# Kernel tuning notes

Measured on AMD Instinct MI355X. Metric: run time of the kernel, lower is better.

## Reference

```python
import jax, jax.numpy as jnp
import numpy as np

N_NODES = 100000
N_PAIRS = 1600000
F = 64
H = 4
D = F // H  # head dim = 16


def setup_inputs() -> dict:
    key = jax.random.key(0)
    ks = jax.random.split(key, 9)
    x = jax.random.normal(ks[0], (N_NODES, F), dtype=jnp.float32)
    w_ij = jax.random.normal(ks[1], (N_PAIRS, F), dtype=jnp.float32)
    phi_r_cut = jax.random.uniform(ks[2], (N_PAIRS,), dtype=jnp.float32)
    pair_mask = jnp.ones((N_PAIRS,), dtype=jnp.float32)
    Wq = jax.random.normal(ks[3], (H, D, D), dtype=jnp.float32) / np.sqrt(D)
    Wk = jax.random.normal(ks[4], (H, D, D), dtype=jnp.float32) / np.sqrt(D)
    Wv = jax.random.normal(ks[5], (H, D, D), dtype=jnp.float32) / np.sqrt(D)
    idx_i = jnp.sort(jax.random.randint(ks[6], (N_PAIRS,), 0, N_NODES)).astype(jnp.int64)
    idx_j = jax.random.randint(ks[7], (N_PAIRS,), 0, N_NODES).astype(jnp.int64)
    return {"x": x, "w_ij": w_ij, "phi_r_cut": phi_r_cut, "pair_mask": pair_mask,
            "Wq": Wq, "Wk": Wk, "Wv": Wv, "idx_i": idx_i, "idx_j": idx_j}


def reference(x, w_ij, phi_r_cut, pair_mask, Wq, Wk, Wv, idx_i, idx_j):
    n, f = x.shape
    h, d, _ = Wq.shape
    xh = x.reshape(n, h, d)            # (n, H, D) head split
    wh = w_ij.reshape(-1, h, d)        # (p, H, D)
    # per-head projections (Dense with no bias: x @ kernel), then gather by edge
    q_i = jnp.einsum('nhd,hde->nhe', xh, Wq)[idx_i]   # (p, H, D)
    k_j = jnp.einsum('nhd,hde->nhe', xh, Wk)[idx_j]   # (p, H, D)
    alpha = (q_i * wh * k_j).sum(axis=-1) / jnp.sqrt(jnp.asarray(d, x.dtype))  # (p, H)
    alpha = alpha * (pair_mask * phi_r_cut)[:, None]  # safe_scale with cutoff * mask
    v_j = jnp.einsum('nhd,hde->nhe', xh, Wv)[idx_j]   # (p, H, D)
    out = jax.ops.segment_sum(alpha[..., None] * v_j, idx_i, num_segments=n)  # (n, H, D)
    return out.reshape(n, f)
```

## Files before the change

kernel.cpp:

```cpp
#include <hip/hip_runtime.h>
#include <stdint.h>

#define N_NODES_C 100000
#define N_PAIRS_C 1600000
#define FDIM 64
#define HH 4
#define DD 16

__global__ __launch_bounds__(256) void qkv_kernel(
    const float* __restrict__ x,
    const float* __restrict__ Wq,
    const float* __restrict__ Wk,
    const float* __restrict__ Wv,
    float* __restrict__ q,
    float* __restrict__ k,
    float* __restrict__ v)
{
    __shared__ float sWq[HH * DD * DD];
    __shared__ float sWk[HH * DD * DD];
    __shared__ float sWv[HH * DD * DD];
    for (int t = threadIdx.x; t < HH * DD * DD; t += 256) {
        sWq[t] = Wq[t];
        sWk[t] = Wk[t];
        sWv[t] = Wv[t];
    }
    __syncthreads();

    int gid = blockIdx.x * 256 + threadIdx.x;
    int n = gid >> 2;
    int h = gid & 3;
    if (n >= N_NODES_C) return;

    const float* xp = x + (int64_t)n * FDIM + h * DD;
    float xr[DD];
#pragma unroll
    for (int d0 = 0; d0 < DD; d0 += 4) {
        float4 t4 = *reinterpret_cast<const float4*>(xp + d0);
        xr[d0 + 0] = t4.x; xr[d0 + 1] = t4.y; xr[d0 + 2] = t4.z; xr[d0 + 3] = t4.w;
    }

    float qo[DD], ko[DD], vo[DD];
#pragma unroll
    for (int e = 0; e < DD; e++) { qo[e] = 0.f; ko[e] = 0.f; vo[e] = 0.f; }

    const float* wqh = sWq + h * DD * DD;
    const float* wkh = sWk + h * DD * DD;
    const float* wvh = sWv + h * DD * DD;
#pragma unroll
    for (int d = 0; d < DD; d++) {
        float xv = xr[d];
#pragma unroll
        for (int e = 0; e < DD; e++) {
            qo[e] = fmaf(xv, wqh[d * DD + e], qo[e]);
            ko[e] = fmaf(xv, wkh[d * DD + e], ko[e]);
            vo[e] = fmaf(xv, wvh[d * DD + e], vo[e]);
        }
    }

    int64_t base = (int64_t)n * FDIM + h * DD;
#pragma unroll
    for (int e0 = 0; e0 < DD; e0 += 4) {
        *reinterpret_cast<float4*>(q + base + e0) = make_float4(qo[e0], qo[e0+1], qo[e0+2], qo[e0+3]);
        *reinterpret_cast<float4*>(k + base + e0) = make_float4(ko[e0], ko[e0+1], ko[e0+2], ko[e0+3]);
        *reinterpret_cast<float4*>(v + base + e0) = make_float4(vo[e0], vo[e0+1], vo[e0+2], vo[e0+3]);
    }
}

__global__ __launch_bounds__(256) void pair_kernel(
    const float* __restrict__ q,
    const float* __restrict__ k,
    const float* __restrict__ v,
    const float* __restrict__ w_ij,
    const float* __restrict__ phi,
    const float* __restrict__ mask,
    const int*  __restrict__ idx_i,
    const int*  __restrict__ idx_j,
    float* __restrict__ out,
    int pairs_per_wave)
{
    int wave = (blockIdx.x * blockDim.x + threadIdx.x) >> 6;
    int lane = threadIdx.x & 63;
    int64_t start = (int64_t)wave * pairs_per_wave;
    if (start >= N_PAIRS_C) return;
    int64_t end = start + pairs_per_wave;
    if (end > N_PAIRS_C) end = N_PAIRS_C;

    float acc = 0.f;
    float qv = 0.f;
    int cur_i = -1;

    for (int64_t p = start; p < end; ++p) {
        int i = idx_i[p];
        if (i != cur_i) {
            if (cur_i >= 0) atomicAdd(&out[(int64_t)cur_i * FDIM + lane], acc);
            acc = 0.f;
            cur_i = i;
            qv = q[(int64_t)i * FDIM + lane];
        }
        int j = idx_j[p];
        float wv = w_ij[p * FDIM + lane];
        float kv = k[(int64_t)j * FDIM + lane];
        float vv = v[(int64_t)j * FDIM + lane];
        float s  = phi[p] * mask[p];

        float r = qv * wv * kv;
        r += __shfl_xor(r, 1);
        r += __shfl_xor(r, 2);
        r += __shfl_xor(r, 4);
        r += __shfl_xor(r, 8);
        float alpha = r * 0.25f * s;

        acc = fmaf(alpha, vv, acc);
    }
    if (cur_i >= 0) atomicAdd(&out[(int64_t)cur_i * FDIM + lane], acc);
}

extern "C" void kernel_launch(void* const* d_in, const int* in_sizes, int n_in,
                              void* d_out, int out_size, void* d_ws, size_t ws_size,
                              hipStream_t stream) {
    const float* x       = (const float*)d_in[0];
    const float* w_ij    = (const float*)d_in[1];
    const float* phi     = (const float*)d_in[2];
    const float* mask    = (const float*)d_in[3];
    const float* Wq      = (const float*)d_in[4];
    const float* Wk      = (const float*)d_in[5];
    const float* Wv      = (const float*)d_in[6];
    const int*   idx_i   = (const int*)d_in[7];
    const int*   idx_j   = (const int*)d_in[8];
    float* out = (float*)d_out;

    float* q = (float*)d_ws;
    float* k = q + (int64_t)N_NODES_C * FDIM;
    float* v = k + (int64_t)N_NODES_C * FDIM;

    hipMemsetAsync(d_out, 0, (size_t)out_size * sizeof(float), stream);

    int qkv_blocks = (N_NODES_C * HH + 255) / 256;
    qkv_kernel<<<qkv_blocks, 256, 0, stream>>>(x, Wq, Wk, Wv, q, k, v);

    const int n_waves = 8192;
    int pairs_per_wave = (N_PAIRS_C + n_waves - 1) / n_waves;
    pair_kernel<<<n_waves / 4, 256, 0, stream>>>(q, k, v, w_ij, phi, mask,
                                                 idx_i, idx_j, out, pairs_per_wave);
}
```

Baseline: 830.1 us.

## Process each pair with 16-lane float4 groups and software-prefetch next pairs

The pair kernel now assigns 16 lanes per pair-stream instead of a full 64-lane wave, with each lane handling a float4 of features. This gives 4x more independent pair streams and vectorized loads. It also adds a two-stage software pipeline that prefetches indices, scales and w/k/v rows for upcoming pairs to hide gather latency. The QKV kernel pads its shared weight arrays per head to reduce LDS bank conflicts. The cost is more registers and four scalar atomics per lane per flush.

```diff
diff --git a/kernel.cpp b/kernel.cpp
--- a/kernel.cpp
+++ b/kernel.cpp
@@ -16,13 +16,13 @@
     float* __restrict__ k,
     float* __restrict__ v)
 {
-    __shared__ float sWq[HH * DD * DD];
-    __shared__ float sWk[HH * DD * DD];
-    __shared__ float sWv[HH * DD * DD];
+    __shared__ float sWq[HH][DD * DD + 8];
+    __shared__ float sWk[HH][DD * DD + 8];
+    __shared__ float sWv[HH][DD * DD + 8];
     for (int t = threadIdx.x; t < HH * DD * DD; t += 256) {
-        sWq[t] = Wq[t];
-        sWk[t] = Wk[t];
-        sWv[t] = Wv[t];
+        sWq[t >> 8][t & 255] = Wq[t];
+        sWk[t >> 8][t & 255] = Wk[t];
+        sWv[t >> 8][t & 255] = Wv[t];
     }
     __syncthreads();
 
@@ -43,9 +43,9 @@
 #pragma unroll
     for (int e = 0; e < DD; e++) { qo[e] = 0.f; ko[e] = 0.f; vo[e] = 0.f; }
 
-    const float* wqh = sWq + h * DD * DD;
-    const float* wkh = sWk + h * DD * DD;
-    const float* wvh = sWv + h * DD * DD;
+    const float* wqh = sWq[h];
+    const float* wkh = sWk[h];
+    const float* wvh = sWv[h];
 #pragma unroll
     for (int d = 0; d < DD; d++) {
         float xv = xr[d];
@@ -76,43 +76,85 @@
     const int*  __restrict__ idx_i,
     const int*  __restrict__ idx_j,
     float* __restrict__ out,
-    int pairs_per_wave)
+    int pairs_per_group)
 {
-    int wave = (blockIdx.x * blockDim.x + threadIdx.x) >> 6;
-    int lane = threadIdx.x & 63;
-    int64_t start = (int64_t)wave * pairs_per_wave;
+    int gid = blockIdx.x * 256 + threadIdx.x;
+    int grp = gid >> 4;
+    int m   = threadIdx.x & 15;
+
+    int64_t start = (int64_t)grp * pairs_per_group;
     if (start >= N_PAIRS_C) return;
-    int64_t end = start + pairs_per_wave;
+    int64_t end = start + pairs_per_group;
     if (end > N_PAIRS_C) end = N_PAIRS_C;
 
-    float acc = 0.f;
-    float qv = 0.f;
-    int cur_i = -1;
+    const float4* w4p = reinterpret_cast<const float4*>(w_ij);
+    const float4* q4p = reinterpret_cast<const float4*>(q);
+    const float4* k4p = reinterpret_cast<const float4*>(k);
+    const float4* v4p = reinterpret_cast<const float4*>(v);
+
+    int64_t p1 = (start + 1 < end) ? start + 1 : end - 1;
+    int   i_a = idx_i[start];
+    int   j_a = idx_j[start];
+    float s_a = phi[start] * mask[start];
+    int   i_b = idx_i[p1];
+    int   j_b = idx_j[p1];
+    float s_b = phi[p1] * mask[p1];
+
+    float4 w_a = w4p[start * DD + m];
+    float4 k_a = k4p[(int64_t)j_a * DD + m];
+    float4 v_a = v4p[(int64_t)j_a * DD + m];
+
+    float4 q4  = q4p[(int64_t)i_a * DD + m];
+    int cur_i  = i_a;
+    float4 acc = make_float4(0.f, 0.f, 0.f, 0.f);
 
     for (int64_t p = start; p < end; ++p) {
-        int i = idx_i[p];
-        if (i != cur_i) {
-            if (cur_i >= 0) atomicAdd(&out[(int64_t)cur_i * FDIM + lane], acc);
-            acc = 0.f;
-            cur_i = i;
-            qv = q[(int64_t)i * FDIM + lane];
+        int64_t p2 = (p + 2 < end) ? p + 2 : end - 1;
+        int   i_c = idx_i[p2];
+        int   j_c = idx_j[p2];
+        float s_c = phi[p2] * mask[p2];
+
+        int64_t pn = (p + 1 < end) ? p + 1 : end - 1;
+        float4 w_b = w4p[pn * DD + m];
+        float4 k_b = k4p[(int64_t)j_b * DD + m];
+        float4 v_b = v4p[(int64_t)j_b * DD + m];
+
+        if (i_a != cur_i) {
+            int64_t ob = (int64_t)cur_i * FDIM + m * 4;
+            atomicAdd(&out[ob + 0], acc.x);
+            atomicAdd(&out[ob + 1], acc.y);
+            atomicAdd(&out[ob + 2], acc.z);
+            atomicAdd(&out[ob + 3], acc.w);
+            acc = make_float4(0.f, 0.f, 0.f, 0.f);
+            q4 = q4p[(int64_t)i_a * DD + m];
+            cur_i = i_a;
         }
-        int j = idx_j[p];
-        float wv = w_ij[p * FDIM + lane];
-        float kv = k[(int64_t)j * FDIM + lane];
-        float vv = v[(int64_t)j * FDIM + lane];
-        float s  = phi[p] * mask[p];
 
-        float r = qv * wv * kv;
+        float r = q4.x * w_a.x * k_a.x
+                + q4.y * w_a.y * k_a.y
+                + q4.z * w_a.z * k_a.z
+                + q4.w * w_a.w * k_a.w;
         r += __shfl_xor(r, 1);
         r += __shfl_xor(r, 2);
-        r += __shfl_xor(r, 4);
-        r += __shfl_xor(r, 8);
-        float alpha = r * 0.25f * s;
+        float alpha = r * 0.25f * s_a;
 
-        acc = fmaf(alpha, vv, acc);
+        acc.x = fmaf(alpha, v_a.x, acc.x);
+        acc.y = fmaf(alpha, v_a.y, acc.y);
+        acc.z = fmaf(alpha, v_a.z, acc.z);
+        acc.w = fmaf(alpha, v_a.w, acc.w);
+
+        i_a = i_b; j_a = j_b; s_a = s_b;
+        w_a = w_b; k_a = k_b; v_a = v_b;
+        i_b = i_c; j_b = j_c; s_b = s_c;
     }
-    if (cur_i >= 0) atomicAdd(&out[(int64_t)cur_i * FDIM + lane], acc);
+
+    {
+        int64_t ob = (int64_t)cur_i * FDIM + m * 4;
+        atomicAdd(&out[ob + 0], acc.x);
+        atomicAdd(&out[ob + 1], acc.y);
+        atomicAdd(&out[ob + 2], acc.z);
+        atomicAdd(&out[ob + 3], acc.w);
+    }
 }
 
 extern "C" void kernel_launch(void* const* d_in, const int* in_sizes, int n_in,
@@ -138,8 +180,8 @@
     int qkv_blocks = (N_NODES_C * HH + 255) / 256;
     qkv_kernel<<<qkv_blocks, 256, 0, stream>>>(x, Wq, Wk, Wv, q, k, v);
 
-    const int n_waves = 8192;
-    int pairs_per_wave = (N_PAIRS_C + n_waves - 1) / n_waves;
-    pair_kernel<<<n_waves / 4, 256, 0, stream>>>(q, k, v, w_ij, phi, mask,
-                                                 idx_i, idx_j, out, pairs_per_wave);
+    const int n_groups = 32768;
+    int pairs_per_group = (N_PAIRS_C + n_groups - 1) / n_groups;
+    pair_kernel<<<n_groups / 16, 256, 0, stream>>>(q, k, v, w_ij, phi, mask,
+                                                   idx_i, idx_j, out, pairs_per_group);
 }
```

Result: faster. 723.0 us (-12.9%).
